# Performance work log

Hardware: AMD Instinct MI355X
Metric: run time of the kernel (lower is better)

Reference implementation:

```python
import jax, jax.numpy as jnp
import numpy as np

OUT_F = 4096
IN_F = 4096
GROUP = 128
NUM_GROUPS = IN_F // GROUP  # 32
PACKED = (OUT_F * IN_F + 3) // 4  # 4194304


def setup_inputs() -> dict:
    key = jax.random.key(0)
    k1, k2, k3, k4, k5 = jax.random.split(key, 5)
    x = jax.random.normal(k1, (4, 2048, IN_F), dtype=jnp.float32)
    weight_packed = jax.random.randint(k2, (PACKED,), 0, 256, dtype=jnp.int32)
    scales = jax.random.uniform(k3, (OUT_F, NUM_GROUPS), dtype=jnp.float32)
    zeros = jax.random.normal(k4, (OUT_F, NUM_GROUPS), dtype=jnp.float32)
    bias = jax.random.normal(k5, (OUT_F,), dtype=jnp.float32)
    return {"x": x, "weight_packed": weight_packed, "scales": scales,
            "zeros": zeros, "bias": bias}


def _dequant_weight(weight_packed, scales, zeros, dtype):
    shifts = jnp.array([0, 2, 4, 6], dtype=jnp.int32)
    w_int = (weight_packed[:, None] >> shifts[None, :]) & 3  # [PACKED, 4]
    w_int = w_int.reshape(-1)[: OUT_F * IN_F].reshape(OUT_F, NUM_GROUPS, GROUP)
    # Per-group dequant: w = q * scale + zero
    w = w_int.astype(dtype) * scales[:, :, None] + zeros[:, :, None]
    return w.reshape(OUT_F, IN_F)


def reference(x, weight_packed, scales, zeros, bias):
    w = _dequant_weight(weight_packed, scales, zeros, x.dtype)  # [out, in]
    # F.linear: x @ w.T + bias
    out = jnp.einsum('bsi,oi->bso', x, w) + bias
    return out
```

## Files before the change

### kernel.cpp

```cpp
#include <hip/hip_runtime.h>
#include <hip/hip_bf16.h>
#include <cstdint>
#include <cstddef>

#define KDIM 4096
#define NDIM 4096
#define NG 32
#define GRP 128

typedef __attribute__((ext_vector_type(8))) short short8;
typedef __attribute__((ext_vector_type(8))) __bf16 bf16x8;
typedef __attribute__((ext_vector_type(4))) float f32x4;
typedef __attribute__((ext_vector_type(4))) int i32x4;

__device__ __forceinline__ unsigned short bf16_rne(float f) {
    unsigned int u = __builtin_bit_cast(unsigned int, f);
    u += 0x7fffu + ((u >> 16) & 1u);
    return (unsigned short)(u >> 16);
}

__device__ __forceinline__ void gload16(const void* g, void* l) {
    __builtin_amdgcn_global_load_lds(
        (const __attribute__((address_space(1))) unsigned int*)g,
        (__attribute__((address_space(3))) unsigned int*)l,
        16, 0, 0);
}

__global__ void prep_kernel(const float* __restrict__ x, const int* __restrict__ wp,
                            const float* __restrict__ scales, const float* __restrict__ zeros,
                            signed char* __restrict__ xq, signed char* __restrict__ wq,
                            unsigned short* __restrict__ Sb, float* __restrict__ arow,
                            unsigned short* __restrict__ zb, float* __restrict__ st,
                            int nbx, int nbw) {
    const int b = blockIdx.x;
    const int t = threadIdx.x;
    if (b < nbx) {
        __shared__ float red[256];
        __shared__ float gs[256];
        const float4* xr = (const float4*)(x + (size_t)b * KDIM);
        float4 v[4];
        float mx = 0.f, sum = 0.f;
#pragma unroll
        for (int j = 0; j < 4; ++j) {
            v[j] = xr[t * 4 + j];
            mx = fmaxf(mx, fmaxf(fmaxf(fabsf(v[j].x), fabsf(v[j].y)),
                                 fmaxf(fabsf(v[j].z), fabsf(v[j].w))));
            sum += v[j].x + v[j].y + v[j].z + v[j].w;
        }
        red[t] = mx; gs[t] = sum;
        __syncthreads();
        for (int s = 128; s > 0; s >>= 1) {
            if (t < s) red[t] = fmaxf(red[t], red[t + s]);
            __syncthreads();
        }
        const float amax = red[0];
        const float inv = (amax > 0.f) ? 127.f / amax : 0.f;
        union { signed char c[16]; i32x4 q; } o;
#pragma unroll
        for (int j = 0; j < 4; ++j) {
            o.c[4 * j + 0] = (signed char)(int)rintf(v[j].x * inv);
            o.c[4 * j + 1] = (signed char)(int)rintf(v[j].y * inv);
            o.c[4 * j + 2] = (signed char)(int)rintf(v[j].z * inv);
            o.c[4 * j + 3] = (signed char)(int)rintf(v[j].w * inv);
        }
        ((i32x4*)(xq + (size_t)b * KDIM))[t] = o.q;
        if (t < NG) {
            float s8 = 0.f;
#pragma unroll
            for (int j = 0; j < 8; ++j) s8 += gs[t * 8 + j];
            Sb[(size_t)b * NG + t] = bf16_rne(s8);
        }
        if (t == 0) arow[b] = amax * (1.f / 127.f);
    } else if (b < nbx + nbw) {
        long i = (long)(b - nbx) * 256 + t;
        int4 p = ((const int4*)wp)[i];
        union { signed char c[16]; i32x4 q; } o;
#pragma unroll
        for (int j = 0; j < 4; ++j) {
            o.c[j]      = (signed char)((p.x >> (2 * j)) & 3);
            o.c[4 + j]  = (signed char)((p.y >> (2 * j)) & 3);
            o.c[8 + j]  = (signed char)((p.z >> (2 * j)) & 3);
            o.c[12 + j] = (signed char)((p.w >> (2 * j)) & 3);
        }
        ((i32x4*)wq)[i] = o.q;
    } else {
        long i = (long)(b - nbx - nbw) * 256 + t;
        int oo = (int)(i >> 5), g = (int)(i & 31);
        zb[i] = bf16_rne(zeros[i]);
        st[(size_t)g * NDIM + oo] = scales[i];
    }
}


#define WGBAR \
    __builtin_amdgcn_sched_barrier(0); \
    __builtin_amdgcn_s_barrier(); \
    __builtin_amdgcn_sched_barrier(0);

#define VMCNT(N) \
    __builtin_amdgcn_sched_barrier(0); \
    asm volatile("s_waitcnt vmcnt(" #N ")" ::: "memory"); \
    __builtin_amdgcn_sched_barrier(0);

__global__ __launch_bounds__(512, 2) void gemm_i8(const signed char* __restrict__ A,
                                                  const signed char* __restrict__ B,
                                                  const unsigned short* __restrict__ Sb,
                                                  const float* __restrict__ arow,
                                                  const unsigned short* __restrict__ zb,
                                                  const float* __restrict__ st,
                                                  const float* __restrict__ bias,
                                                  float* __restrict__ C) {
    __shared__ __align__(16) signed char sm[133120];

    const int tid = threadIdx.x;
    const int w64 = tid >> 6;
    const int lane = tid & 63;

    const int nwg = gridDim.x;
    const int chunk = nwg >> 3;
    const int s_id = (blockIdx.x & 7) * chunk + (blockIdx.x >> 3);
    const int nm = nwg >> 4;
    const int bm = s_id % nm;
    const int bn = s_id / nm;
    const int row0 = bm * 256;
    const int col0 = bn * 256;

    const int wr = w64 >> 2;
    const int wc = w64 & 3;

    const int srow = tid >> 3;
    const int sswz = 16 * ((tid & 7) ^ (srow & 7));
    const signed char* srcA = A + (size_t)(row0 + srow) * KDIM + sswz;
    const signed char* srcB = B + (size_t)(col0 + srow) * KDIM + sswz;
    const float* srcS = st + col0 + (lane << 2);

    const int lr = lane & 15;
    const int lk4 = lane >> 4;
    const int l7 = lane & 7;
    const int sw0 = 16 * (lk4 ^ l7);
    const int sw1 = 16 * ((4 + lk4) ^ l7);
    const int aBase = (wr * 128 + lr) * 128;
    const int bBase = 32768 + (wc * 64 + lr) * 128;

    f32x4 acc[8][4] = {};

    auto stageA = [&](int hh, int tile, int db) {
        const signed char* g = srcA + (size_t)hh * 128 * KDIM + (size_t)tile * 128;
        signed char* l = &sm[db * 66560 + hh * 16384 + w64 * 1024];
        gload16(g, l);
        gload16(g + (size_t)64 * KDIM, l + 8192);
    };
    auto stageB = [&](int hh, int tile, int db) {
        const signed char* g = srcB + (size_t)hh * 128 * KDIM + (size_t)tile * 128;
        signed char* l = &sm[db * 66560 + 32768 + hh * 16384 + w64 * 1024];
        gload16(g, l);
        gload16(g + (size_t)64 * KDIM, l + 8192);
    };
    auto stageS = [&](int tile, int db) {
        gload16(srcS + (size_t)tile * NDIM, &sm[db * 66560 + 65536]);
    };

    const int NT = KDIM / GRP;

    stageA(0, 0, 0); stageA(1, 0, 0); stageB(0, 0, 0); stageB(1, 0, 0); stageS(0, 0);
    stageA(0, 1, 1); stageA(1, 1, 1); stageB(0, 1, 1); stageB(1, 1, 1); stageS(1, 1);
    VMCNT(9)
    WGBAR

    for (int t = 0; t < NT; ++t) {
        const int d = t & 1;
        const int dOff = d * 66560;
        const int t2 = (t + 2 < NT) ? t + 2 : t;

        i32x4 bQ[4][2];
        float s4[4];
#pragma unroll
        for (int ni = 0; ni < 4; ++ni) {
            bQ[ni][0] = *(const i32x4*)&sm[dOff + bBase + ni * 2048 + sw0];
            bQ[ni][1] = *(const i32x4*)&sm[dOff + bBase + ni * 2048 + sw1];
        }
#pragma unroll
        for (int ni = 0; ni < 4; ++ni)
            s4[ni] = *(const float*)&sm[dOff + 65536 + (wc * 64 + ni * 16 + lr) * 4];

        __builtin_amdgcn_s_setprio(1);
#pragma unroll
        for (int mh = 0; mh < 2; ++mh) {
            i32x4 aF[4][2];
#pragma unroll
            for (int mi = 0; mi < 4; ++mi) {
                aF[mi][0] = *(const i32x4*)&sm[dOff + aBase + (mh * 4 + mi) * 2048 + sw0];
                aF[mi][1] = *(const i32x4*)&sm[dOff + aBase + (mh * 4 + mi) * 2048 + sw1];
            }
#pragma unroll
            for (int mi = 0; mi < 4; ++mi)
#pragma unroll
                for (int ni = 0; ni < 4; ++ni) {
                    i32x4 ai = __builtin_amdgcn_mfma_i32_16x16x64_i8(
                        aF[mi][0], bQ[ni][0], (i32x4){0, 0, 0, 0}, 0, 0, 0);
                    ai = __builtin_amdgcn_mfma_i32_16x16x64_i8(
                        aF[mi][1], bQ[ni][1], ai, 0, 0, 0);
#pragma unroll
                    for (int r = 0; r < 4; ++r)
                        acc[mh * 4 + mi][ni][r] += s4[ni] * (float)ai[r];
                }
        }
        __builtin_amdgcn_s_setprio(0);

        WGBAR
        stageA(0, t2, d); stageA(1, t2, d); stageB(0, t2, d); stageB(1, t2, d); stageS(t2, d);
        VMCNT(9)
        WGBAR
    }

    __builtin_amdgcn_sched_barrier(0);
    asm volatile("s_waitcnt vmcnt(0) lgkmcnt(0)" ::: "memory");
    __builtin_amdgcn_sched_barrier(0);

    float am[8][4];
#pragma unroll
    for (int m = 0; m < 8; ++m)
#pragma unroll
        for (int r = 0; r < 4; ++r)
            am[m][r] = arow[row0 + wr * 128 + m * 16 + lk4 * 4 + r];
#pragma unroll
    for (int m = 0; m < 8; ++m)
#pragma unroll
        for (int n = 0; n < 4; ++n)
#pragma unroll
            for (int r = 0; r < 4; ++r)
                acc[m][n][r] *= am[m][r];

    short8 aS[8], bZ[4];
#pragma unroll
    for (int m = 0; m < 8; ++m)
        aS[m] = *(const short8*)&Sb[(size_t)(row0 + wr * 128 + m * 16 + lr) * NG + lk4 * 8];
#pragma unroll
    for (int n = 0; n < 4; ++n)
        bZ[n] = *(const short8*)&zb[(size_t)(col0 + wc * 64 + n * 16 + lr) * NG + lk4 * 8];
#pragma unroll
    for (int m = 0; m < 8; ++m)
#pragma unroll
        for (int n = 0; n < 4; ++n)
            acc[m][n] = __builtin_amdgcn_mfma_f32_16x16x32_bf16(
                __builtin_bit_cast(bf16x8, aS[m]), __builtin_bit_cast(bf16x8, bZ[n]),
                acc[m][n], 0, 0, 0);

#pragma unroll
    for (int m = 0; m < 8; ++m) {
#pragma unroll
        for (int n = 0; n < 4; ++n) {
            int col = col0 + wc * 64 + n * 16 + lr;
            float bz = bias[col];
#pragma unroll
            for (int r = 0; r < 4; ++r) {
                int row = row0 + wr * 128 + m * 16 + lk4 * 4 + r;
                C[(size_t)row * NDIM + col] = acc[m][n][r] + bz;
            }
        }
    }
}

__global__ void fallback_kernel(const float* __restrict__ x, const int* __restrict__ wp,
                                const float* __restrict__ scales, const float* __restrict__ zeros,
                                const float* __restrict__ bias, float* __restrict__ out) {
    int o = blockIdx.x * 256 + threadIdx.x;
    int m = blockIdx.y;
    __shared__ float xs[KDIM];
    for (int i = threadIdx.x; i < KDIM; i += 256) xs[i] = x[(size_t)m * KDIM + i];
    __syncthreads();
    float acc = 0.f;
    for (int g = 0; g < 32; ++g) {
        float s = scales[o * 32 + g], z = zeros[o * 32 + g];
        float aq = 0.f, ax = 0.f;
        for (int j = 0; j < 32; ++j) {
            int p = wp[o * 1024 + g * 32 + j];
            int kb = g * 128 + j * 4;
#pragma unroll
            for (int q = 0; q < 4; ++q) {
                float xv = xs[kb + q];
                aq += xv * (float)((p >> (2 * q)) & 3);
                ax += xv;
            }
        }
        acc += s * aq + z * ax;
    }
    out[(size_t)m * NDIM + o] = acc + bias[o];
}

extern "C" void kernel_launch(void* const* d_in, const int* in_sizes, int n_in,
                              void* d_out, int out_size, void* d_ws, size_t ws_size,
                              hipStream_t stream) {
    const float* x      = (const float*)d_in[0];
    const int*   wp     = (const int*)d_in[1];
    const float* scales = (const float*)d_in[2];
    const float* zeros  = (const float*)d_in[3];
    const float* bias   = (const float*)d_in[4];
    float* out = (float*)d_out;

    const long M = (long)in_sizes[0] / KDIM;
    const long PACKED = (long)in_sizes[1];

    const size_t xq_off = 0;
    const size_t wq_off = (size_t)M * KDIM;
    const size_t Sb_off = wq_off + (size_t)NDIM * KDIM;
    const size_t ar_off = Sb_off + (size_t)M * NG * 2;
    const size_t zb_off = ar_off + (size_t)M * 4;
    const size_t st_off = zb_off + (size_t)NDIM * NG * 2;
    const size_t need   = st_off + (size_t)NG * NDIM * 4;

    if (ws_size >= need && (M % 256) == 0) {
        signed char* xq = (signed char*)d_ws + xq_off;
        signed char* wq = (signed char*)d_ws + wq_off;
        unsigned short* Sb = (unsigned short*)((char*)d_ws + Sb_off);
        float* ar = (float*)((char*)d_ws + ar_off);
        unsigned short* zb = (unsigned short*)((char*)d_ws + zb_off);
        float* st = (float*)((char*)d_ws + st_off);

        int nbx = (int)M;
        int nbw = (int)((NDIM * (long)KDIM / 16) / 256);
        int nbz = (int)((NDIM * (long)NG) / 256);
        prep_kernel<<<nbx + nbw + nbz, 256, 0, stream>>>(x, wp, scales, zeros,
                                                         xq, wq, Sb, ar, zb, st, nbx, nbw);
        int nwg = (int)(M / 256) * (NDIM / 256);
        gemm_i8<<<nwg, 512, 0, stream>>>(xq, wq, Sb, ar, zb, st, bias, out);
    } else {
        dim3 grid(NDIM / 256, M);
        fallback_kernel<<<grid, 256, 0, stream>>>(x, wp, scales, zeros, bias, out);
    }
}
```

Baseline: 237.5 us.

## Shrink GEMM tile to 256x128 with 64-wide K steps for higher occupancy

The int8 GEMM tile drops from 256x256 with 128-wide K slices to 256x128 with 64-wide K slices. Each wave now holds 4x4 accumulators instead of 8x4, and LDS use falls from about 130 KB to 50 KB, so launch bounds ask for 4 blocks per CU instead of 2. The grid doubles and the LDS swizzle and staging are rebuilt for 64-byte rows. This trades per-tile data reuse and barrier count (twice as many K iterations, each with two barriers) for more resident waves to hide latency.

```diff
diff --git a/kernel.cpp b/kernel.cpp
--- a/kernel.cpp
+++ b/kernel.cpp
@@ -92,6 +92,8 @@
 }
 
 
+#define SMBUF 25600
+
 #define WGBAR \
     __builtin_amdgcn_sched_barrier(0); \
     __builtin_amdgcn_s_barrier(); \
@@ -102,7 +104,7 @@
     asm volatile("s_waitcnt vmcnt(" #N ")" ::: "memory"); \
     __builtin_amdgcn_sched_barrier(0);
 
-__global__ __launch_bounds__(512, 2) void gemm_i8(const signed char* __restrict__ A,
+__global__ __launch_bounds__(512, 4) void gemm_i8(const signed char* __restrict__ A,
                                                   const signed char* __restrict__ B,
                                                   const unsigned short* __restrict__ Sb,
                                                   const float* __restrict__ arow,
@@ -110,7 +112,7 @@
                                                   const float* __restrict__ st,
                                                   const float* __restrict__ bias,
                                                   float* __restrict__ C) {
-    __shared__ __align__(16) signed char sm[133120];
+    __shared__ __align__(16) signed char sm[2 * SMBUF];
 
     const int tid = threadIdx.x;
     const int w64 = tid >> 6;
@@ -119,97 +121,81 @@
     const int nwg = gridDim.x;
     const int chunk = nwg >> 3;
     const int s_id = (blockIdx.x & 7) * chunk + (blockIdx.x >> 3);
-    const int nm = nwg >> 4;
+    const int nm = nwg >> 5;
     const int bm = s_id % nm;
     const int bn = s_id / nm;
     const int row0 = bm * 256;
-    const int col0 = bn * 256;
-
-    const int wr = w64 >> 2;
-    const int wc = w64 & 3;
-
-    const int srow = tid >> 3;
-    const int sswz = 16 * ((tid & 7) ^ (srow & 7));
+    const int col0 = bn * 128;
+
+    const int wr = w64 >> 1;
+    const int wc = w64 & 1;
+
+    const int srow = tid >> 2;
+    const int sswz = 16 * ((tid & 3) ^ ((tid >> 3) & 3));
     const signed char* srcA = A + (size_t)(row0 + srow) * KDIM + sswz;
     const signed char* srcB = B + (size_t)(col0 + srow) * KDIM + sswz;
-    const float* srcS = st + col0 + (lane << 2);
+    const float* srcS = st + col0 + ((lane & 31) << 2);
 
     const int lr = lane & 15;
     const int lk4 = lane >> 4;
-    const int l7 = lane & 7;
-    const int sw0 = 16 * (lk4 ^ l7);
-    const int sw1 = 16 * ((4 + lk4) ^ l7);
-    const int aBase = (wr * 128 + lr) * 128;
-    const int bBase = 32768 + (wc * 64 + lr) * 128;
-
-    f32x4 acc[8][4] = {};
-
-    auto stageA = [&](int hh, int tile, int db) {
-        const signed char* g = srcA + (size_t)hh * 128 * KDIM + (size_t)tile * 128;
-        signed char* l = &sm[db * 66560 + hh * 16384 + w64 * 1024];
-        gload16(g, l);
-        gload16(g + (size_t)64 * KDIM, l + 8192);
+    const int sw = 16 * (lk4 ^ ((lr >> 1) & 3));
+    const int aBase = (wr * 64 + lr) * 64;
+    const int bBase = 16384 + (wc * 64 + lr) * 64;
+
+    f32x4 acc[4][4] = {};
+
+    auto stage = [&](int tile, int db) {
+        const signed char* gA = srcA + (size_t)tile * 64;
+        const signed char* gB = srcB + (size_t)tile * 64;
+        signed char* lA = &sm[db * SMBUF + w64 * 1024];
+        signed char* lB = &sm[db * SMBUF + 16384 + w64 * 1024];
+        gload16(gA, lA);
+        gload16(gA + (size_t)128 * KDIM, lA + 8192);
+        gload16(gB, lB);
+        gload16(srcS + (size_t)(tile >> 1) * NDIM, &sm[db * SMBUF + 24576]);
     };
-    auto stageB = [&](int hh, int tile, int db) {
-        const signed char* g = srcB + (size_t)hh * 128 * KDIM + (size_t)tile * 128;
-        signed char* l = &sm[db * 66560 + 32768 + hh * 16384 + w64 * 1024];
-        gload16(g, l);
-        gload16(g + (size_t)64 * KDIM, l + 8192);
-    };
-    auto stageS = [&](int tile, int db) {
-        gload16(srcS + (size_t)tile * NDIM, &sm[db * 66560 + 65536]);
-    };
-
-    const int NT = KDIM / GRP;
-
-    stageA(0, 0, 0); stageA(1, 0, 0); stageB(0, 0, 0); stageB(1, 0, 0); stageS(0, 0);
-    stageA(0, 1, 1); stageA(1, 1, 1); stageB(0, 1, 1); stageB(1, 1, 1); stageS(1, 1);
-    VMCNT(9)
+
+    const int NT = KDIM / 64;
+
+    stage(0, 0);
+    stage(1, 1);
+    VMCNT(4)
     WGBAR
 
     for (int t = 0; t < NT; ++t) {
         const int d = t & 1;
-        const int dOff = d * 66560;
+        const int dOff = d * SMBUF;
         const int t2 = (t + 2 < NT) ? t + 2 : t;
 
-        i32x4 bQ[4][2];
+        i32x4 bQ[4];
         float s4[4];
 #pragma unroll
-        for (int ni = 0; ni < 4; ++ni) {
-            bQ[ni][0] = *(const i32x4*)&sm[dOff + bBase + ni * 2048 + sw0];
-            bQ[ni][1] = *(const i32x4*)&sm[dOff + bBase + ni * 2048 + sw1];
-        }
-#pragma unroll
-        for (int ni = 0; ni < 4; ++ni)
-            s4[ni] = *(const float*)&sm[dOff + 65536 + (wc * 64 + ni * 16 + lr) * 4];
+        for (int n = 0; n < 4; ++n)
+            bQ[n] = *(const i32x4*)&sm[dOff + bBase + n * 1024 + sw];
+#pragma unroll
+        for (int n = 0; n < 4; ++n)
+            s4[n] = *(const float*)&sm[dOff + 24576 + (wc * 64 + n * 16 + lr) * 4];
 
         __builtin_amdgcn_s_setprio(1);
-#pragma unroll
-        for (int mh = 0; mh < 2; ++mh) {
-            i32x4 aF[4][2];
-#pragma unroll
-            for (int mi = 0; mi < 4; ++mi) {
-                aF[mi][0] = *(const i32x4*)&sm[dOff + aBase + (mh * 4 + mi) * 2048 + sw0];
-                aF[mi][1] = *(const i32x4*)&sm[dOff + aBase + (mh * 4 + mi) * 2048 + sw1];
+        i32x4 aF[4];
+#pragma unroll
+        for (int m = 0; m < 4; ++m)
+            aF[m] = *(const i32x4*)&sm[dOff + aBase + m * 1024 + sw];
+#pragma unroll
+        for (int m = 0; m < 4; ++m)
+#pragma unroll
+            for (int n = 0; n < 4; ++n) {
+                i32x4 ai = __builtin_amdgcn_mfma_i32_16x16x64_i8(
+                    aF[m], bQ[n], (i32x4){0, 0, 0, 0}, 0, 0, 0);
+#pragma unroll
+                for (int r = 0; r < 4; ++r)
+                    acc[m][n][r] += s4[n] * (float)ai[r];
             }
-#pragma unroll
-            for (int mi = 0; mi < 4; ++mi)
-#pragma unroll
-                for (int ni = 0; ni < 4; ++ni) {
-                    i32x4 ai = __builtin_amdgcn_mfma_i32_16x16x64_i8(
-                        aF[mi][0], bQ[ni][0], (i32x4){0, 0, 0, 0}, 0, 0, 0);
-                    ai = __builtin_amdgcn_mfma_i32_16x16x64_i8(
-                        aF[mi][1], bQ[ni][1], ai, 0, 0, 0);
-#pragma unroll
-                    for (int r = 0; r < 4; ++r)
-                        acc[mh * 4 + mi][ni][r] += s4[ni] * (float)ai[r];
-                }
-        }
         __builtin_amdgcn_s_setprio(0);
 
         WGBAR
-        stageA(0, t2, d); stageA(1, t2, d); stageB(0, t2, d); stageB(1, t2, d); stageS(t2, d);
-        VMCNT(9)
+        stage(t2, d);
+        VMCNT(4)
         WGBAR
     }
 
@@ -217,29 +203,29 @@
     asm volatile("s_waitcnt vmcnt(0) lgkmcnt(0)" ::: "memory");
     __builtin_amdgcn_sched_barrier(0);
 
-    float am[8][4];
-#pragma unroll
-    for (int m = 0; m < 8; ++m)
+    float am[4][4];
+#pragma unroll
+    for (int m = 0; m < 4; ++m)
 #pragma unroll
         for (int r = 0; r < 4; ++r)
-            am[m][r] = arow[row0 + wr * 128 + m * 16 + lk4 * 4 + r];
-#pragma unroll
-    for (int m = 0; m < 8; ++m)
+            am[m][r] = arow[row0 + wr * 64 + m * 16 + lk4 * 4 + r];
+#pragma unroll
+    for (int m = 0; m < 4; ++m)
 #pragma unroll
         for (int n = 0; n < 4; ++n)
 #pragma unroll
             for (int r = 0; r < 4; ++r)
                 acc[m][n][r] *= am[m][r];
 
-    short8 aS[8], bZ[4];
-#pragma unroll
-    for (int m = 0; m < 8; ++m)
-        aS[m] = *(const short8*)&Sb[(size_t)(row0 + wr * 128 + m * 16 + lr) * NG + lk4 * 8];
+    short8 aS[4], bZ[4];
+#pragma unroll
+    for (int m = 0; m < 4; ++m)
+        aS[m] = *(const short8*)&Sb[(size_t)(row0 + wr * 64 + m * 16 + lr) * NG + lk4 * 8];
 #pragma unroll
     for (int n = 0; n < 4; ++n)
         bZ[n] = *(const short8*)&zb[(size_t)(col0 + wc * 64 + n * 16 + lr) * NG + lk4 * 8];
 #pragma unroll
-    for (int m = 0; m < 8; ++m)
+    for (int m = 0; m < 4; ++m)
 #pragma unroll
         for (int n = 0; n < 4; ++n)
             acc[m][n] = __builtin_amdgcn_mfma_f32_16x16x32_bf16(
@@ -247,14 +233,14 @@
                 acc[m][n], 0, 0, 0);
 
 #pragma unroll
-    for (int m = 0; m < 8; ++m) {
+    for (int m = 0; m < 4; ++m) {
 #pragma unroll
         for (int n = 0; n < 4; ++n) {
             int col = col0 + wc * 64 + n * 16 + lr;
             float bz = bias[col];
 #pragma unroll
             for (int r = 0; r < 4; ++r) {
-                int row = row0 + wr * 128 + m * 16 + lk4 * 4 + r;
+                int row = row0 + wr * 64 + m * 16 + lk4 * 4 + r;
                 C[(size_t)row * NDIM + col] = acc[m][n][r] + bz;
             }
         }
@@ -322,7 +308,7 @@
         int nbz = (int)((NDIM * (long)NG) / 256);
         prep_kernel<<<nbx + nbw + nbz, 256, 0, stream>>>(x, wp, scales, zeros,
                                                          xq, wq, Sb, ar, zb, st, nbx, nbw);
-        int nwg = (int)(M / 256) * (NDIM / 256);
+        int nwg = (int)(M / 256) * (NDIM / 128);
         gemm_i8<<<nwg, 512, 0, stream>>>(xq, wq, Sb, ar, zb, st, bias, out);
     } else {
         dim3 grid(NDIM / 256, M);
```

Measured after the change: 275.1 us. +15.9%, slower.
